# Kernel tuning notes

Measured on AMD Instinct MI355X. Metric: run time of the kernel, lower is better.

Reference implementation:

```python
import jax, jax.numpy as jnp
import numpy as np

N_NODES = 50000
N_EDGES = 800000
D_IN = 64
D_OUT = 64

def setup_inputs() -> dict:
    key = jax.random.key(0)
    k1, k2, k3, k4 = jax.random.split(key, 4)
    x = jax.random.normal(k1, (N_NODES, D_IN), dtype=jnp.float32)
    # Linear(in, out, bias=False): weight shape [out, in], Kaiming-uniform-ish scale
    bound = 1.0 / np.sqrt(D_IN)
    W = jax.random.uniform(k2, (D_OUT, D_IN), dtype=jnp.float32, minval=-bound, maxval=bound)
    src = jax.random.randint(k3, (N_EDGES,), 0, N_NODES, dtype=jnp.int32)
    dst = jax.random.randint(k4, (N_EDGES,), 0, N_NODES, dtype=jnp.int32)
    return {"x": x, "W": W, "src": src, "dst": dst}

def reference(x, W, src, dst):
    # update_all(copy_src, sum): for each edge (s, d), add x[s] into node d
    agg = jax.ops.segment_sum(x[src], dst, num_segments=N_NODES)  # [N, D_IN]
    # linear1 (bias=False); dropout is identity at inference
    h = jnp.einsum('nd,od->no', agg, W)  # [N, D_OUT]
    h = jax.nn.relu(h)
    # is_normalize=False -> skip L2 normalize; residual adds input node features
    return h + x
```

## Files before the change

### kernel.cpp

```cpp
#include <hip/hip_runtime.h>

#define D 64
#define NCHUNK 256
#define CAP 48

__device__ __forceinline__ float bflo(unsigned u) { return __uint_as_float(u << 16); }
__device__ __forceinline__ float bfhi(unsigned u) { return __uint_as_float(u & 0xffff0000u); }
__device__ __forceinline__ unsigned short f2bf(float f) {
    unsigned b = __float_as_uint(f);
    return (unsigned short)((b + 0x7fffu + ((b >> 16) & 1u)) >> 16);
}

__global__ __launch_bounds__(256) void hist_kernel(
    const int* __restrict__ dst, unsigned int* __restrict__ bh32, int n_nodes, int ne) {
    __shared__ unsigned int lds[12544];
    const int tid = threadIdx.x;
    const int nw = (n_nodes + 3) >> 2;
    const int c = blockIdx.x;
    const int csz = (ne + NCHUNK - 1) / NCHUNK;
    const int e0 = c * csz, e1 = min(e0 + csz, ne);
    for (int i = tid; i < nw; i += 256) lds[i] = 0;
    __syncthreads();
    for (int e = e0 + tid; e < e1; e += 256) {
        const int d = dst[e];
        atomicAdd(&lds[d >> 2], 1u << ((d & 3) * 8));
    }
    __syncthreads();
    unsigned int* bh = bh32 + (size_t)c * nw;
    for (int i = tid; i < nw; i += 256) bh[i] = lds[i];
}

__global__ __launch_bounds__(256) void colscan_gemm_kernel(
    const float* __restrict__ x, const float* __restrict__ W,
    unsigned char* __restrict__ bh8, int* __restrict__ counts,
    unsigned short* __restrict__ ybf, int n_nodes, int ne, int csb) {
    __shared__ float4 lds4[2048];
    const int tid = threadIdx.x;
    if ((int)blockIdx.x < csb) {
        const int d = blockIdx.x * 256 + tid;
        if (d >= n_nodes) return;
        const size_t npad4 = (size_t)((n_nodes + 3) >> 2) * 4;
        int acc = 0;
        for (int c0 = 0; c0 < NCHUNK; c0 += 8) {
            unsigned char v[8];
#pragma unroll
            for (int k = 0; k < 8; ++k) v[k] = bh8[(size_t)(c0 + k) * npad4 + d];
#pragma unroll
            for (int k = 0; k < 8; ++k) {
                bh8[(size_t)(c0 + k) * npad4 + d] = (unsigned char)acc;
                acc += v[k];
            }
        }
        counts[d] = acc;
        return;
    }
    float4* As4 = lds4;
    float4* Wc4 = lds4 + 1024;
    const float4* W4 = (const float4*)W;
    for (int i = tid; i < 1024; i += 256) {
        const int kc = i >> 6, o = i & 63;
        Wc4[i] = W4[o * 16 + kc];
    }
    const int grp = (int)blockIdx.x - csb;
    const int base = grp * 64;
    const float4* x4 = (const float4*)x;
#pragma unroll
    for (int r = 0; r < 4; ++r) {
        const int i = r * 256 + tid;
        const int row = i >> 4, col = i & 15;
        const int gidx = base * 16 + i;
        if (gidx < n_nodes * 16) As4[row * 16 + (col ^ (row & 15))] = x4[gidx];
    }
    __syncthreads();
    const int q = tid & 15, g = tid >> 4;
    float acc[4][4];
#pragma unroll
    for (int j = 0; j < 4; ++j)
#pragma unroll
        for (int i = 0; i < 4; ++i) acc[j][i] = 0.f;
    for (int kc = 0; kc < 16; ++kc) {
        float4 a[4], wv[4];
#pragma unroll
        for (int j = 0; j < 4; ++j) {
            const int rr = g * 4 + j;
            a[j] = As4[rr * 16 + (kc ^ (rr & 15))];
        }
#pragma unroll
        for (int i = 0; i < 4; ++i) wv[i] = Wc4[kc * 64 + q + 16 * i];
#pragma unroll
        for (int j = 0; j < 4; ++j)
#pragma unroll
            for (int i = 0; i < 4; ++i) {
                acc[j][i] = fmaf(a[j].x, wv[i].x, acc[j][i]);
                acc[j][i] = fmaf(a[j].y, wv[i].y, acc[j][i]);
                acc[j][i] = fmaf(a[j].z, wv[i].z, acc[j][i]);
                acc[j][i] = fmaf(a[j].w, wv[i].w, acc[j][i]);
            }
    }
#pragma unroll
    for (int j = 0; j < 4; ++j) {
        const int n = base + g * 4 + j;
        if (n >= n_nodes) break;
#pragma unroll
        for (int i = 0; i < 4; ++i)
            ybf[(size_t)n * D + q + 16 * i] = f2bf(acc[j][i]);
    }
}

__global__ __launch_bounds__(256) void place_kernel(
    const int* __restrict__ src, const int* __restrict__ dst,
    const unsigned int* __restrict__ bh32, int* __restrict__ esrc,
    int n_nodes, int ne) {
    __shared__ unsigned int lw[12544];
    const int c = blockIdx.x;
    const int csz = (ne + NCHUNK - 1) / NCHUNK;
    const int e0 = c * csz, e1 = min(e0 + csz, ne);
    const int nw = (n_nodes + 3) >> 2;
    const unsigned int* bh = bh32 + (size_t)c * nw;
    for (int i = threadIdx.x; i < nw; i += 256) lw[i] = bh[i];
    __syncthreads();
    for (int e = e0 + threadIdx.x; e < e1; e += 256) {
        const int d = dst[e];
        const unsigned old = atomicAdd(&lw[d >> 2], 1u << ((d & 3) * 8));
        const int slot = (old >> ((d & 3) * 8)) & 0xff;
        if (slot < CAP) esrc[d * CAP + slot] = src[e];
    }
}

__global__ void gather_kernel(const int* __restrict__ counts, const int* __restrict__ esrc,
                              const unsigned short* __restrict__ ybf,
                              const float* __restrict__ x, float* __restrict__ out,
                              int n_nodes) {
    const int tid = threadIdx.x;
    const int w = tid >> 6, lane = tid & 63;
    const int g = lane >> 3, m = lane & 7;
    const uint4* Y4 = (const uint4*)ybf;
    const float4* x4 = (const float4*)x;
    float4* out4 = (float4*)out;
    const int nWaves = gridDim.x * 4;

    int n = blockIdx.x * 4 + w;
    int c = 0, s_all = 0;
    if (n < n_nodes) {
        c = min(counts[n], CAP);
        s_all = (lane < c) ? esrc[n * CAP + lane] : 0;
    }
    while (n < n_nodes) {
        const int n2 = n + nWaves;
        int c2 = 0, s2 = 0;
        if (n2 < n_nodes) {
            c2 = min(counts[n2], CAP);
            s2 = (lane < c2) ? esrc[n2 * CAP + lane] : 0;
        }
        float acc[8] = {0.f, 0.f, 0.f, 0.f, 0.f, 0.f, 0.f, 0.f};
        for (int j = 0; j < c; j += 8) {
            const int e = j + g;
            const int s = __shfl(s_all, e);
            if (e < c) {
                const uint4 v = Y4[(size_t)s * 8 + m];
                acc[0] += bflo(v.x); acc[1] += bfhi(v.x);
                acc[2] += bflo(v.y); acc[3] += bfhi(v.y);
                acc[4] += bflo(v.z); acc[5] += bfhi(v.z);
                acc[6] += bflo(v.w); acc[7] += bfhi(v.w);
            }
        }
#pragma unroll
        for (int k = 0; k < 8; ++k) {
            acc[k] += __shfl_xor(acc[k], 8);
            acc[k] += __shfl_xor(acc[k], 16);
            acc[k] += __shfl_xor(acc[k], 32);
        }
        if (lane < 8) {
            const float4 xa = x4[(size_t)n * 16 + lane * 2];
            const float4 xb = x4[(size_t)n * 16 + lane * 2 + 1];
            float4 oa, ob;
            oa.x = fmaxf(acc[0], 0.f) + xa.x;
            oa.y = fmaxf(acc[1], 0.f) + xa.y;
            oa.z = fmaxf(acc[2], 0.f) + xa.z;
            oa.w = fmaxf(acc[3], 0.f) + xa.w;
            ob.x = fmaxf(acc[4], 0.f) + xb.x;
            ob.y = fmaxf(acc[5], 0.f) + xb.y;
            ob.z = fmaxf(acc[6], 0.f) + xb.z;
            ob.w = fmaxf(acc[7], 0.f) + xb.w;
            out4[(size_t)n * 16 + lane * 2] = oa;
            out4[(size_t)n * 16 + lane * 2 + 1] = ob;
        }
        n = n2; c = c2; s_all = s2;
    }
}

extern "C" void kernel_launch(void* const* d_in, const int* in_sizes, int n_in,
                              void* d_out, int out_size, void* d_ws, size_t ws_size,
                              hipStream_t stream) {
    const float* x = (const float*)d_in[0];
    const float* W = (const float*)d_in[1];
    const int* src = (const int*)d_in[2];
    const int* dst = (const int*)d_in[3];
    float* out = (float*)d_out;

    const int n_nodes = in_sizes[0] / D;
    const int n_edges = in_sizes[2];
    const int nw = (n_nodes + 3) >> 2;

    unsigned int* bh32 = (unsigned int*)d_ws;
    int* counts = (int*)(bh32 + (size_t)NCHUNK * nw);
    int* esrc = counts + n_nodes;
    unsigned short* ybf = (unsigned short*)(esrc + (size_t)n_nodes * CAP);

    const int csb = (n_nodes + 255) / 256;
    const int ngrp = (n_nodes + 63) / 64;

    hist_kernel<<<NCHUNK, 256, 0, stream>>>(dst, bh32, n_nodes, n_edges);
    colscan_gemm_kernel<<<csb + ngrp, 256, 0, stream>>>(
        x, W, (unsigned char*)bh32, counts, ybf, n_nodes, n_edges, csb);
    place_kernel<<<NCHUNK, 256, 0, stream>>>(src, dst, bh32, esrc, n_nodes, n_edges);
    gather_kernel<<<2048, 256, 0, stream>>>(counts, esrc, ybf, x, out, n_nodes);
}
```

Baseline: 131.9 us.

## Split the feature GEMM across the histogram and column-scan launches, 512-thread blocks

The dense x·W GEMM moves out of the column-scan kernel alone and is split in half. One half runs in a new combined histogram+GEMM kernel, so CUs left idle by the 256 histogram blocks do GEMM work. The other half stays with the column scan. Block size goes from 256 to 512 for hist, colscan, GEMM (now 128 rows per block) and place, and shared memory is resized to fit both uses. The cost is higher LDS use per block and larger blocks, which may reduce occupancy or raise LDS atomic contention in the histogram.

```diff
diff --git a/kernel.cpp b/kernel.cpp
--- a/kernel.cpp
+++ b/kernel.cpp
@@ -11,62 +11,21 @@
     return (unsigned short)((b + 0x7fffu + ((b >> 16) & 1u)) >> 16);
 }
 
-__global__ __launch_bounds__(256) void hist_kernel(
-    const int* __restrict__ dst, unsigned int* __restrict__ bh32, int n_nodes, int ne) {
-    __shared__ unsigned int lds[12544];
-    const int tid = threadIdx.x;
-    const int nw = (n_nodes + 3) >> 2;
-    const int c = blockIdx.x;
-    const int csz = (ne + NCHUNK - 1) / NCHUNK;
-    const int e0 = c * csz, e1 = min(e0 + csz, ne);
-    for (int i = tid; i < nw; i += 256) lds[i] = 0;
-    __syncthreads();
-    for (int e = e0 + tid; e < e1; e += 256) {
-        const int d = dst[e];
-        atomicAdd(&lds[d >> 2], 1u << ((d & 3) * 8));
-    }
-    __syncthreads();
-    unsigned int* bh = bh32 + (size_t)c * nw;
-    for (int i = tid; i < nw; i += 256) bh[i] = lds[i];
-}
-
-__global__ __launch_bounds__(256) void colscan_gemm_kernel(
-    const float* __restrict__ x, const float* __restrict__ W,
-    unsigned char* __restrict__ bh8, int* __restrict__ counts,
-    unsigned short* __restrict__ ybf, int n_nodes, int ne, int csb) {
-    __shared__ float4 lds4[2048];
-    const int tid = threadIdx.x;
-    if ((int)blockIdx.x < csb) {
-        const int d = blockIdx.x * 256 + tid;
-        if (d >= n_nodes) return;
-        const size_t npad4 = (size_t)((n_nodes + 3) >> 2) * 4;
-        int acc = 0;
-        for (int c0 = 0; c0 < NCHUNK; c0 += 8) {
-            unsigned char v[8];
-#pragma unroll
-            for (int k = 0; k < 8; ++k) v[k] = bh8[(size_t)(c0 + k) * npad4 + d];
-#pragma unroll
-            for (int k = 0; k < 8; ++k) {
-                bh8[(size_t)(c0 + k) * npad4 + d] = (unsigned char)acc;
-                acc += v[k];
-            }
-        }
-        counts[d] = acc;
-        return;
-    }
+__device__ __forceinline__ void gemm_body(
+    int grp, int tid, float4* lds4, const float* __restrict__ x,
+    const float* __restrict__ W, unsigned short* __restrict__ ybf, int n_nodes) {
     float4* As4 = lds4;
-    float4* Wc4 = lds4 + 1024;
+    float4* Wc4 = lds4 + 2048;
     const float4* W4 = (const float4*)W;
-    for (int i = tid; i < 1024; i += 256) {
+    for (int i = tid; i < 1024; i += 512) {
         const int kc = i >> 6, o = i & 63;
         Wc4[i] = W4[o * 16 + kc];
     }
-    const int grp = (int)blockIdx.x - csb;
-    const int base = grp * 64;
+    const int base = grp * 128;
     const float4* x4 = (const float4*)x;
 #pragma unroll
     for (int r = 0; r < 4; ++r) {
-        const int i = r * 256 + tid;
+        const int i = r * 512 + tid;
         const int row = i >> 4, col = i & 15;
         const int gidx = base * 16 + i;
         if (gidx < n_nodes * 16) As4[row * 16 + (col ^ (row & 15))] = x4[gidx];
@@ -107,7 +66,60 @@
     }
 }
 
-__global__ __launch_bounds__(256) void place_kernel(
+__global__ __launch_bounds__(512) void hist_gemm_kernel(
+    const int* __restrict__ dst, unsigned int* __restrict__ bh32,
+    const float* __restrict__ x, const float* __restrict__ W,
+    unsigned short* __restrict__ ybf, int n_nodes, int ne) {
+    __shared__ float4 lds4[3136];
+    const int tid = threadIdx.x;
+    if ((int)blockIdx.x < NCHUNK) {
+        unsigned int* lds = (unsigned int*)lds4;
+        const int nw = (n_nodes + 3) >> 2;
+        const int c = blockIdx.x;
+        const int csz = (ne + NCHUNK - 1) / NCHUNK;
+        const int e0 = c * csz, e1 = min(e0 + csz, ne);
+        for (int i = tid; i < nw; i += 512) lds[i] = 0;
+        __syncthreads();
+        for (int e = e0 + tid; e < e1; e += 512) {
+            const int d = dst[e];
+            atomicAdd(&lds[d >> 2], 1u << ((d & 3) * 8));
+        }
+        __syncthreads();
+        unsigned int* bh = bh32 + (size_t)c * nw;
+        for (int i = tid; i < nw; i += 512) bh[i] = lds[i];
+        return;
+    }
+    gemm_body((int)blockIdx.x - NCHUNK, tid, lds4, x, W, ybf, n_nodes);
+}
+
+__global__ __launch_bounds__(512) void colscan_gemm_kernel(
+    const float* __restrict__ x, const float* __restrict__ W,
+    unsigned char* __restrict__ bh8, int* __restrict__ counts,
+    unsigned short* __restrict__ ybf, int n_nodes, int ne, int csb, int grpoff) {
+    __shared__ float4 lds4[3136];
+    const int tid = threadIdx.x;
+    if ((int)blockIdx.x < csb) {
+        const int d = blockIdx.x * 512 + tid;
+        if (d >= n_nodes) return;
+        const size_t npad4 = (size_t)((n_nodes + 3) >> 2) * 4;
+        int acc = 0;
+        for (int c0 = 0; c0 < NCHUNK; c0 += 8) {
+            unsigned char v[8];
+#pragma unroll
+            for (int k = 0; k < 8; ++k) v[k] = bh8[(size_t)(c0 + k) * npad4 + d];
+#pragma unroll
+            for (int k = 0; k < 8; ++k) {
+                bh8[(size_t)(c0 + k) * npad4 + d] = (unsigned char)acc;
+                acc += v[k];
+            }
+        }
+        counts[d] = acc;
+        return;
+    }
+    gemm_body(grpoff + (int)blockIdx.x - csb, tid, lds4, x, W, ybf, n_nodes);
+}
+
+__global__ __launch_bounds__(512) void place_kernel(
     const int* __restrict__ src, const int* __restrict__ dst,
     const unsigned int* __restrict__ bh32, int* __restrict__ esrc,
     int n_nodes, int ne) {
@@ -117,9 +129,9 @@
     const int e0 = c * csz, e1 = min(e0 + csz, ne);
     const int nw = (n_nodes + 3) >> 2;
     const unsigned int* bh = bh32 + (size_t)c * nw;
-    for (int i = threadIdx.x; i < nw; i += 256) lw[i] = bh[i];
+    for (int i = threadIdx.x; i < nw; i += 512) lw[i] = bh[i];
     __syncthreads();
-    for (int e = e0 + threadIdx.x; e < e1; e += 256) {
+    for (int e = e0 + threadIdx.x; e < e1; e += 512) {
         const int d = dst[e];
         const unsigned old = atomicAdd(&lw[d >> 2], 1u << ((d & 3) * 8));
         const int slot = (old >> ((d & 3) * 8)) & 0xff;
@@ -207,12 +219,15 @@
     int* esrc = counts + n_nodes;
     unsigned short* ybf = (unsigned short*)(esrc + (size_t)n_nodes * CAP);
 
-    const int csb = (n_nodes + 255) / 256;
-    const int ngrp = (n_nodes + 63) / 64;
-
-    hist_kernel<<<NCHUNK, 256, 0, stream>>>(dst, bh32, n_nodes, n_edges);
-    colscan_gemm_kernel<<<csb + ngrp, 256, 0, stream>>>(
-        x, W, (unsigned char*)bh32, counts, ybf, n_nodes, n_edges, csb);
-    place_kernel<<<NCHUNK, 256, 0, stream>>>(src, dst, bh32, esrc, n_nodes, n_edges);
+    const int ngrp = (n_nodes + 127) / 128;
+    const int g1 = (ngrp + 1) / 2;
+    const int g2 = ngrp - g1;
+    const int csb = (n_nodes + 511) / 512;
+
+    hist_gemm_kernel<<<NCHUNK + g1, 512, 0, stream>>>(
+        dst, bh32, x, W, ybf, n_nodes, n_edges);
+    colscan_gemm_kernel<<<csb + g2, 512, 0, stream>>>(
+        x, W, (unsigned char*)bh32, counts, ybf, n_nodes, n_edges, csb, g1);
+    place_kernel<<<NCHUNK, 512, 0, stream>>>(src, dst, bh32, esrc, n_nodes, n_edges);
     gather_kernel<<<2048, 256, 0, stream>>>(counts, esrc, ybf, x, out, n_nodes);
 }
```

New measurement: 132.2 us. No clear change (+0.3%).
